# Kernel tuning notes

Hardware: AMD Instinct MI355X
Metric: run time of the kernel (lower is better)

## Reference

```python
import jax, jax.numpy as jnp
import numpy as np

WAVE_LEN = 1000.0

def rank_embedding(rank_dim, feat_dim):
    half = feat_dim // 2
    dim_mat = jnp.arange(half, dtype=jnp.float32) / half
    inv = 1.0 / jnp.power(WAVE_LEN, dim_mat)            # [half]
    mul = jnp.arange(rank_dim, dtype=jnp.float32)[:, None] * inv[None, :]  # [K, half]
    return jnp.concatenate([jnp.sin(mul), jnp.cos(mul)], axis=-1)          # [K, feat_dim]

def setup_inputs() -> dict:
    key = jax.random.key(0)
    ks = jax.random.split(key, 16)
    K, NS, NC, D, DF, H, DK = 2048, 18, 19, 1024, 128, 16, 64
    s = 0.02
    return {
        "size_scores": jax.random.normal(ks[0], (1, K, NS), jnp.float32),
        "size_residuals_normalized": jax.random.normal(ks[1], (1, K, NS, 3), jnp.float32),
        "sem_cls_scores": jax.random.normal(ks[2], (K, NC), jnp.float32),
        "appearance_features": jax.random.normal(ks[3], (K, D), jnp.float32),
        "mean_size_arr": jax.random.uniform(ks[4], (NS, 3), jnp.float32, 0.1, 1.0),
        "w_rank": jax.random.normal(ks[5], (D, DF), jnp.float32) * s,
        "b_rank": jnp.zeros((DF,), jnp.float32),
        "w_roi": jax.random.normal(ks[6], (D, DF), jnp.float32) * s,
        "b_roi": jnp.zeros((DF,), jnp.float32),
        "Wq": jax.random.normal(ks[7], (H, DF, DK), jnp.float32) * s,
        "Wk": jax.random.normal(ks[8], (H, DF, DK), jnp.float32) * s,
        "Wv": jax.random.normal(ks[9], (H, D, DK), jnp.float32) * s,
        "w_logit": jax.random.normal(ks[10], (D, 1), jnp.float32) * s,
        "b_logit": jnp.zeros((1,), jnp.float32),
    }

def reference(size_scores, size_residuals_normalized, sem_cls_scores,
              appearance_features, mean_size_arr,
              w_rank, b_rank, w_roi, b_roi, Wq, Wk, Wv, w_logit, b_logit):
    K, D = appearance_features.shape
    # --- predicted box size: gather residual for argmax size class ---
    pred_size_class = jnp.argmax(size_scores, axis=-1)                     # [1,K]
    size_residuals = size_residuals_normalized * mean_size_arr[None, None] # [1,K,NS,3]
    pred_size_residual = jnp.take_along_axis(
        size_residuals, pred_size_class[..., None, None], axis=2)[:, :, 0, :]  # [1,K,3]
    psc = pred_size_class[0]                                               # [K]
    box_size = mean_size_arr[psc] + pred_size_residual[0]                  # [K,3]
    # --- semantic class prob ---
    prob_all = jax.nn.softmax(sem_cls_scores, axis=-1)                     # [K,NC]
    prob = jnp.max(prob_all, axis=-1)                                      # [K]
    prob_argmax = jnp.argmax(prob_all, axis=-1)                            # [K]
    cls_bbox = box_size                                                    # [K,3]
    # --- background masking (jit-friendly analog of nonzero filtering):
    # background (class 0) proposals get key -1 so they sort to the end with score 0.
    fg = prob_argmax > 0
    sort_key = jnp.where(fg, prob, -1.0)
    order = jnp.argsort(-sort_key)                                         # descending
    sorted_prob = jnp.where(fg[order], prob[order], 0.0)                   # [K]
    sorted_labels = prob_argmax[order]                                     # [K]
    sorted_cls_bboxes = cls_bbox[order]                                    # [K,3]
    sorted_features = appearance_features[order]                           # [K,D]
    # --- rank embedding + roi embedding ---
    emb = rank_embedding(K, D)                                             # [K,D]
    nms_rank = emb @ w_rank + b_rank                                       # [K,DF]
    roi = sorted_features @ w_roi + b_roi                                  # [K,DF]
    e = nms_rank + roi                                                     # [K,DF]
    # --- relation-module self-attention: Q/K from embedding, V from features ---
    dk = Wq.shape[-1]
    q = jnp.einsum('kd,hde->hke', e, Wq)                                   # [H,K,dk]
    k = jnp.einsum('kd,hde->hke', e, Wk)
    scores = jnp.einsum('hke,hme->hkm', q, k) / jnp.sqrt(jnp.float32(dk))  # [H,K,K]
    attn = jax.nn.softmax(scores, axis=-1)
    v = jnp.einsum('kf,hfe->hke', sorted_features, Wv)                     # [H,K,dk]
    o = jnp.einsum('hkm,hme->hke', attn, v)                                # [H,K,dk]
    o = jnp.transpose(o, (1, 0, 2)).reshape(K, -1)                         # [K,D]
    attn_out = sorted_features + o                                         # residual
    # --- nms logit ---
    logit = attn_out @ w_logit + b_logit                                   # [K,1]
    s1 = jax.nn.sigmoid(logit).reshape(-1)
    nms_scores = s1 * sorted_prob
    return nms_scores, sorted_labels - 1, sorted_cls_bboxes
```

## Files before the change

kernel.cpp:

```cpp
#include <hip/hip_runtime.h>

#define KP 2048
#define DD 1024
#define DF 128
#define NH 16
#define DKK 64
#define NSS 18
#define NCC 19
#define NCH 2
#define CHUNK 1024
#define SPLK 16

typedef __attribute__((ext_vector_type(8))) short short8;
typedef __attribute__((ext_vector_type(4))) short short4_t;
typedef __attribute__((ext_vector_type(4))) float f32x4;

__device__ __forceinline__ short f2bf(float x){
    unsigned u = __float_as_uint(x);
    u += 0x7fffu + ((u >> 16) & 1u);
    return (short)(u >> 16);
}

__device__ __forceinline__ void gl2lds16(const void* g, void* l){
    __builtin_amdgcn_global_load_lds((const __attribute__((address_space(1))) void*)g,
                                     (__attribute__((address_space(3))) void*)l, 16, 0, 0);
}

__global__ __launch_bounds__(256) void prep_convw_kernel(const float* __restrict__ size_scores,
        const float* __restrict__ srn, const float* __restrict__ sem,
        const float* __restrict__ mean,
        const float* __restrict__ w_rank, const float* __restrict__ w_roi,
        const float* __restrict__ Wq, const float* __restrict__ Wk,
        const float* __restrict__ Wv, const float* __restrict__ w_logit,
        float* __restrict__ box, int* __restrict__ label,
        double* __restrict__ probd, double* __restrict__ keyd,
        short* __restrict__ wcat, short* __restrict__ qkT, short* __restrict__ uT){
    int bid = blockIdx.x, t = threadIdx.x;
    if (bid < 8){
        int k = bid * 256 + t;
        const float* ss = size_scores + k * NSS;
        int psc = 0; float bs = ss[0];
        for (int s = 1; s < NSS; s++){ float v = ss[s]; if (v > bs){ bs = v; psc = s; } }
        for (int c = 0; c < 3; c++){
            float m = mean[psc * 3 + c];
            float r = srn[k * (NSS * 3) + psc * 3 + c];
            box[k * 3 + c] = m + r * m;
        }
        const float* cs = sem + k * NCC;
        double mx = (double)cs[0]; int lab = 0;
        for (int c = 1; c < NCC; c++){ double v = (double)cs[c]; if (v > mx){ mx = v; lab = c; } }
        double sum = 0.0;
        for (int c = 0; c < NCC; c++) sum += exp((double)cs[c] - mx);
        probd[k] = 1.0 / sum;
        label[k] = lab;
        keyd[k]  = (lab > 0) ? (1.0 / sum) : -1.0;
        return;
    }
    int b = bid - 8;
    if (b >= 128){
        int i = b - 128;
        int h = i >> 2;
        int f = ((i & 3) << 8) + t;
        const float* wv = Wv + (size_t)h * DD * DKK + (size_t)f * DKK;
        const float* wlh = w_logit + h * DKK;
        float s = 0.f;
        #pragma unroll
        for (int e = 0; e < DKK; e++) s += wv[e] * wlh[e];
        uT[h * DD + f] = f2bf(s);
        return;
    }
    __shared__ float tile[64][65];
    const float* src; short* dst; int sstride, dstride, r0, c0, doff;
    float scale = 1.0f;
    if (b < 32){        src = w_rank; dst = wcat; sstride = DF; dstride = 2048;
                        r0 = (b >> 1) * 64; c0 = (b & 1) * 64; doff = 0; }
    else if (b < 64){   int i = b - 32; src = w_roi; dst = wcat; sstride = DF; dstride = 2048;
                        r0 = (i >> 1) * 64; c0 = (i & 1) * 64; doff = 1024; }
    else if (b < 96){   int i = b - 64; int h = i >> 1;
                        src = Wq + (size_t)h * DF * DKK; dst = qkT + (size_t)h * DKK * DF;
                        sstride = DKK; dstride = DF; r0 = (i & 1) * 64; c0 = 0; doff = 0;
                        scale = 0.125f; }
    else {              int i = b - 96; int h = i >> 1;
                        src = Wk + (size_t)h * DF * DKK; dst = qkT + (size_t)(1024 + h * DKK) * DF;
                        sstride = DKK; dstride = DF; r0 = (i & 1) * 64; c0 = 0; doff = 0; }
    int tx = t & 63, ty = t >> 6;
    #pragma unroll
    for (int pp = 0; pp < 16; pp++){
        int r = pp * 4 + ty;
        tile[r][tx] = src[(size_t)(r0 + r) * sstride + c0 + tx];
    }
    __syncthreads();
    #pragma unroll
    for (int pp = 0; pp < 16; pp++){
        int r = pp * 4 + ty;
        dst[(size_t)(c0 + r) * dstride + doff + r0 + tx] = f2bf(tile[tx][r] * scale);
    }
}

__global__ __launch_bounds__(256) void rank_af_kernel(const double* __restrict__ keyd,
        const int* __restrict__ label, const double* __restrict__ probd,
        const float* __restrict__ box, const float* __restrict__ app,
        const float* __restrict__ w_logit,
        int* __restrict__ order, float* __restrict__ sprob, float* __restrict__ dotl,
        short* __restrict__ af, unsigned* __restrict__ cnt, float* __restrict__ out){
    int i = blockIdx.x, t = threadIdx.x;
    if (i < 16 && t == 0) cnt[i] = 0;
    __shared__ int redi[4];
    __shared__ float redf[4];
    __shared__ int rks;
    double ki = keyd[i];
    const double2* k2 = (const double2*)keyd;
    int r = 0;
    #pragma unroll
    for (int pp = 0; pp < KP / 2 / 256; pp++){
        int idx2 = pp * 256 + t;
        double2 kj = k2[idx2];
        int j0 = idx2 * 2;
        r += (int)(kj.x > ki) + (int)((kj.x == ki) & (j0 < i));
        r += (int)(kj.y > ki) + (int)((kj.y == ki) & (j0 + 1 < i));
    }
    #pragma unroll
    for (int off = 32; off > 0; off >>= 1) r += __shfl_down(r, off);
    if ((t & 63) == 0) redi[t >> 6] = r;
    __syncthreads();
    if (t == 0){
        int rk = redi[0] + redi[1] + redi[2] + redi[3];
        rks = rk;
        order[rk] = i;
        sprob[rk] = (label[i] > 0) ? (float)probd[i] : 0.f;
        out[KP + rk] = (float)(label[i] - 1);
        out[2 * KP + 3 * rk + 0] = box[i * 3 + 0];
        out[2 * KP + 3 * rk + 1] = box[i * 3 + 1];
        out[2 * KP + 3 * rk + 2] = box[i * 3 + 2];
    }
    __syncthreads();
    int pos = rks;
    float4 v = ((const float4*)(app + (size_t)i * DD))[t];
    float4 wv = ((const float4*)w_logit)[t];
    short4_t gg = { f2bf(v.x), f2bf(v.y), f2bf(v.z), f2bf(v.w) };
    *(short4_t*)(af + (size_t)pos * 2048 + 1024 + t * 4) = gg;
    float partial = v.x * wv.x + v.y * wv.y + v.z * wv.z + v.w * wv.w;
    #pragma unroll
    for (int off = 32; off > 0; off >>= 1) partial += __shfl_down(partial, off);
    if ((t & 63) == 0) redf[t >> 6] = partial;
    short4_t e;
    #pragma unroll
    for (int ii = 0; ii < 4; ii++){
        int j = t * 4 + ii, jj = j & 511;
        float inv = exp2f(-(float)jj * 0.0194644224310197f);
        float arg = (float)pos * inv;
        e[ii] = f2bf((j < 512) ? __sinf(arg) : __cosf(arg));
    }
    *(short4_t*)(af + (size_t)pos * 2048 + t * 4) = e;
    __syncthreads();
    if (t == 0) dotl[pos] = redf[0] + redf[1] + redf[2] + redf[3];
}

__global__ __launch_bounds__(256) void gemm_lds(const short* __restrict__ A,
                                                const short* __restrict__ BT,
                                                void* __restrict__ C,
                                                int lda, int ldb, int N,
                                                int klen, size_t slabstride, int mode){
    int w = threadIdx.x >> 6, lane = threadIdx.x & 63;
    int quad = lane >> 4, l16 = lane & 15;
    int m0 = blockIdx.x * 64, n0 = blockIdx.y * 64;
    int kb = blockIdx.z * klen;

    __shared__ __align__(16) short alds[64 * 64];
    __shared__ __align__(16) short blds[64 * 64];

    int p0 = w * 64 + lane;
    int r0 = p0 >> 3, q0 = ((p0 & 7) ^ (r0 & 7)) * 8;
    int p1 = p0 + 256;
    int r1 = p1 >> 3, q1 = ((p1 & 7) ^ (r1 & 7)) * 8;
    short* adst0 = alds + w * 512;
    short* adst1 = alds + 2048 + w * 512;
    short* bdst0 = blds + w * 512;
    short* bdst1 = blds + 2048 + w * 512;
    const short* asrc0 = A + (size_t)(m0 + r0) * lda + kb + q0;
    const short* asrc1 = A + (size_t)(m0 + r1) * lda + kb + q1;
    const short* bsrc0 = BT + (size_t)(n0 + r0) * ldb + kb + q0;
    const short* bsrc1 = BT + (size_t)(n0 + r1) * ldb + kb + q1;

    f32x4 acc[4];
    for (int c = 0; c < 4; c++) acc[c] = (f32x4){0.f, 0.f, 0.f, 0.f};

    for (int kt = 0; kt < klen; kt += 64){
        __syncthreads();
        gl2lds16(asrc0 + kt, adst0);
        gl2lds16(asrc1 + kt, adst1);
        gl2lds16(bsrc0 + kt, bdst0);
        gl2lds16(bsrc1 + kt, bdst1);
        __syncthreads();
        int arow = w * 16 + l16;
        #pragma unroll
        for (int s = 0; s < 2; s++){
            short8 a = *(const short8*)(alds + arow * 64 + (((s * 4 + quad) ^ (l16 & 7)) * 8));
            #pragma unroll
            for (int c = 0; c < 4; c++){
                int brow = c * 16 + l16;
                short8 b = *(const short8*)(blds + brow * 64 + (((s * 4 + quad) ^ (l16 & 7)) * 8));
                acc[c] = __builtin_amdgcn_mfma_f32_16x16x32_bf16(a, b, acc[c], 0, 0, 0);
            }
        }
    }
    int mrow = m0 + w * 16 + quad * 4;
    #pragma unroll
    for (int c = 0; c < 4; c++){
        #pragma unroll
        for (int r = 0; r < 4; r++){
            size_t idx = (size_t)(mrow + r) * N + n0 + c * 16 + l16;
            if (mode == 2) ((short*)C)[idx] = f2bf(acc[c][r]);
            else ((float*)C + (size_t)blockIdx.z * slabstride)[idx] = acc[c][r];
        }
    }
}

__global__ __launch_bounds__(256) void comb_vw_kernel(const float* __restrict__ es,
        const float* __restrict__ b_rank, const float* __restrict__ b_roi,
        const short* __restrict__ af, const short* __restrict__ uT,
        short* __restrict__ e_bf, float* __restrict__ vwT){
    int bid = blockIdx.x, t = threadIdx.x;
    if (bid < 256){
        int base = (bid * 256 + t) * 4;
        int n = base & (DF - 1);
        float4 s = *(const float4*)(es + base);
        #pragma unroll
        for (int c = 1; c < SPLK; c++){
            float4 tt = *(const float4*)(es + (size_t)c * KP * DF + base);
            s.x += tt.x; s.y += tt.y; s.z += tt.z; s.w += tt.w;
        }
        float4 br = *(const float4*)(b_rank + n);
        float4 bo = *(const float4*)(b_roi + n);
        short4_t o = { f2bf(s.x + br.x + bo.x), f2bf(s.y + br.y + bo.y),
                       f2bf(s.z + br.z + bo.z), f2bf(s.w + br.w + bo.w) };
        *(short4_t*)(e_bf + base) = o;
    } else {
        int vb = bid - 256;
        int w = t >> 6, lane = t & 63, quad = lane >> 4, l16 = lane & 15;
        int m0 = vb * 64 + w * 16;
        f32x4 acc = (f32x4){0.f, 0.f, 0.f, 0.f};
        const short* arow = af + (size_t)(m0 + l16) * 2048 + 1024 + quad * 8;
        const short* brow = uT + (size_t)l16 * DD + quad * 8;
        for (int k0 = 0; k0 < DD; k0 += 32){
            short8 a = *(const short8*)(arow + k0);
            short8 b = *(const short8*)(brow + k0);
            acc = __builtin_amdgcn_mfma_f32_16x16x32_bf16(a, b, acc, 0, 0, 0);
        }
        #pragma unroll
        for (int r = 0; r < 4; r++)
            vwT[(size_t)l16 * KP + m0 + quad * 4 + r] = acc[r];
    }
}

__global__ __launch_bounds__(256, 4) void attn_final_kernel(const short* __restrict__ qk,
        const float* __restrict__ vwT, const float* __restrict__ dotl,
        const float* __restrict__ sprob, const float* __restrict__ b_logit,
        float* __restrict__ pl, float* __restrict__ pwl,
        unsigned* __restrict__ cnt, float* __restrict__ out){
    int qt = blockIdx.x, h = blockIdx.y, ch = blockIdx.z;
    int t = threadIdx.x;
    int w = t >> 6, lane = t & 63, quad = lane >> 4, l16 = lane & 15;
    int qb = qt * 128;

    __shared__ __align__(16) short klds[64 * 64];
    __shared__ int lastf;

    short8 aq[2][2];
    #pragma unroll
    for (int tt = 0; tt < 2; tt++){
        const short* qrow = qk + (size_t)(qb + tt * 64 + w * 16 + l16) * 2048 + h * DKK;
        aq[tt][0] = *(const short8*)(qrow + quad * 8);
        aq[tt][1] = *(const short8*)(qrow + 32 + quad * 8);
    }
    float lpart[2][4] = {{0.f,0.f,0.f,0.f},{0.f,0.f,0.f,0.f}};
    float wpart[2][4] = {{0.f,0.f,0.f,0.f},{0.f,0.f,0.f,0.f}};

    int seg0 = w * 128 + lane;
    int row0 = seg0 >> 3, c80 = (seg0 & 7) ^ (row0 & 7);
    int seg1 = seg0 + 64;
    int row1 = seg1 >> 3, c81 = (seg1 & 7) ^ (row1 & 7);
    short* kl0 = klds + (size_t)(w * 128) * 8;
    short* kl1 = klds + (size_t)(w * 128 + 64) * 8;

    for (int m0 = ch * CHUNK; m0 < (ch + 1) * CHUNK; m0 += 64){
        __syncthreads();
        gl2lds16(qk + (size_t)(m0 + row0) * 2048 + 1024 + h * DKK + c80 * 8, kl0);
        gl2lds16(qk + (size_t)(m0 + row1) * 2048 + 1024 + h * DKK + c81 * 8, kl1);
        float vwv[4];
        #pragma unroll
        for (int c = 0; c < 4; c++)
            vwv[c] = vwT[(size_t)h * KP + m0 + c * 16 + l16];
        __syncthreads();

        #pragma unroll
        for (int tt = 0; tt < 2; tt++){
            #pragma unroll
            for (int c = 0; c < 4; c++){
                int r = c * 16 + l16, sw = r & 7;
                short8 b0 = *(const short8*)(klds + r * 64 + (quad ^ sw) * 8);
                short8 b1 = *(const short8*)(klds + r * 64 + ((quad + 4) ^ sw) * 8);
                f32x4 acc = (f32x4){0.f, 0.f, 0.f, 0.f};
                acc = __builtin_amdgcn_mfma_f32_16x16x32_bf16(aq[tt][0], b0, acc, 0, 0, 0);
                acc = __builtin_amdgcn_mfma_f32_16x16x32_bf16(aq[tt][1], b1, acc, 0, 0, 0);
                #pragma unroll
                for (int rr = 0; rr < 4; rr++){
                    float e = __expf(acc[rr]);
                    lpart[tt][rr] += e;
                    wpart[tt][rr] += e * vwv[c];
                }
            }
        }
    }

    #pragma unroll
    for (int tt = 0; tt < 2; tt++){
        #pragma unroll
        for (int rr = 0; rr < 4; rr++){
            float v = lpart[tt][rr], x = wpart[tt][rr];
            v += __shfl_xor(v, 1); x += __shfl_xor(x, 1);
            v += __shfl_xor(v, 2); x += __shfl_xor(x, 2);
            v += __shfl_xor(v, 4); x += __shfl_xor(x, 4);
            v += __shfl_xor(v, 8); x += __shfl_xor(x, 8);
            lpart[tt][rr] = v; wpart[tt][rr] = x;
        }
        if (l16 == 0){
            int qr0 = qb + tt * 64 + w * 16;
            #pragma unroll
            for (int rr = 0; rr < 4; rr++){
                size_t idx = ((size_t)ch * NH + h) * KP + qr0 + quad * 4 + rr;
                __hip_atomic_store(pl + idx,  lpart[tt][rr], __ATOMIC_RELAXED, __HIP_MEMORY_SCOPE_AGENT);
                __hip_atomic_store(pwl + idx, wpart[tt][rr], __ATOMIC_RELAXED, __HIP_MEMORY_SCOPE_AGENT);
            }
        }
    }
    __syncthreads();
    if (t == 0){
        __threadfence();
        unsigned old = __hip_atomic_fetch_add(cnt + qt, 1u, __ATOMIC_ACQ_REL, __HIP_MEMORY_SCOPE_AGENT);
        lastf = (old == 31);
    }
    __syncthreads();
    if (lastf){
        __threadfence();
        if (t < 128){
            int pos = qb + t;
            float logit = dotl[pos] + b_logit[0];
            #pragma unroll
            for (int hh = 0; hh < NH; hh++){
                size_t i0 = ((size_t)0 * NH + hh) * KP + pos;
                size_t i1 = ((size_t)1 * NH + hh) * KP + pos;
                float l = __hip_atomic_load(pl + i0, __ATOMIC_RELAXED, __HIP_MEMORY_SCOPE_AGENT)
                        + __hip_atomic_load(pl + i1, __ATOMIC_RELAXED, __HIP_MEMORY_SCOPE_AGENT);
                float x = __hip_atomic_load(pwl + i0, __ATOMIC_RELAXED, __HIP_MEMORY_SCOPE_AGENT)
                        + __hip_atomic_load(pwl + i1, __ATOMIC_RELAXED, __HIP_MEMORY_SCOPE_AGENT);
                logit += x / l;
            }
            float s1 = 1.f / (1.f + __expf(-logit));
            out[pos] = s1 * sprob[pos];
        }
    }
}

extern "C" void kernel_launch(void* const* d_in, const int* in_sizes, int n_in,
                              void* d_out, int out_size, void* d_ws, size_t ws_size,
                              hipStream_t stream){
    (void)in_sizes; (void)n_in; (void)out_size; (void)ws_size;
    const float* size_scores = (const float*)d_in[0];
    const float* srn     = (const float*)d_in[1];
    const float* sem     = (const float*)d_in[2];
    const float* app     = (const float*)d_in[3];
    const float* mean    = (const float*)d_in[4];
    const float* w_rank  = (const float*)d_in[5];
    const float* b_rank  = (const float*)d_in[6];
    const float* w_roi   = (const float*)d_in[7];
    const float* b_roi   = (const float*)d_in[8];
    const float* Wq      = (const float*)d_in[9];
    const float* Wk      = (const float*)d_in[10];
    const float* Wv      = (const float*)d_in[11];
    const float* w_logit = (const float*)d_in[12];
    const float* b_logit = (const float*)d_in[13];
    float* out = (float*)d_out;

    char* ws = (char*)d_ws;
    size_t off = 0;
    auto alloc = [&](size_t n) -> char* {
        char* pp = ws + off;
        off = (off + n + 255) & ~(size_t)255;
        return pp;
    };
    float*    box   = (float*)   alloc((size_t)KP * 3 * 4);
    int*      label = (int*)     alloc((size_t)KP * 4);
    double*   probd = (double*)  alloc((size_t)KP * 8);
    double*   keyd  = (double*)  alloc((size_t)KP * 8);
    int*      order = (int*)     alloc((size_t)KP * 4);
    float*    sprob = (float*)   alloc((size_t)KP * 4);
    float*    dotl  = (float*)   alloc((size_t)KP * 4);
    unsigned* cnt   = (unsigned*)alloc(16 * 4);
    short*    wcat  = (short*)   alloc((size_t)DF * 2048 * 2);
    short*    qkT   = (short*)   alloc((size_t)2048 * DF * 2);
    short*    uT    = (short*)   alloc((size_t)NH * DD * 2);
    short*    e_bf  = (short*)   alloc((size_t)KP * DF * 2);
    short*    qk_bf = (short*)   alloc((size_t)KP * 2048 * 2);
    float*    vwT   = (float*)   alloc((size_t)NH * KP * 4);
    float*    pl    = (float*)   alloc((size_t)NCH * NH * KP * 4);
    float*    pwl   = (float*)   alloc((size_t)NCH * NH * KP * 4);
    short*    af    = (short*)   alloc((size_t)KP * 2048 * 2);
    float*    es    = (float*)   alloc((size_t)SPLK * KP * DF * 4);

    prep_convw_kernel<<<200, 256, 0, stream>>>(size_scores, srn, sem, mean,
        w_rank, w_roi, Wq, Wk, Wv, w_logit, box, label, probd, keyd, wcat, qkT, uT);
    rank_af_kernel<<<KP, 256, 0, stream>>>(keyd, label, probd, box, app, w_logit,
        order, sprob, dotl, af, cnt, out);
    gemm_lds<<<dim3(32, 2, SPLK), 256, 0, stream>>>(af, wcat, es, 2048, 2048, DF,
        2048 / SPLK, (size_t)KP * DF, 0);
    comb_vw_kernel<<<288, 256, 0, stream>>>(es, b_rank, b_roi, af, uT, e_bf, vwT);
    gemm_lds<<<dim3(32, 32, 1), 256, 0, stream>>>(e_bf, qkT, qk_bf, DF, DF, 2048, DF, 0, 2);
    attn_final_kernel<<<dim3(16, NH, NCH), 256, 0, stream>>>(qk_bf, vwT, dotl, sprob,
        b_logit, pl, pwl, cnt, out);
}
```

Measured before the change: 154.3 us.

## Split attention key chunks wider, halve split-K, move final reduction to separate kernel

```diff
diff --git a/kernel.cpp b/kernel.cpp
--- a/kernel.cpp
+++ b/kernel.cpp
@@ -7,9 +7,9 @@
 #define DKK 64
 #define NSS 18
 #define NCC 19
-#define NCH 2
-#define CHUNK 1024
-#define SPLK 16
+#define NCH 4
+#define CHUNK 512
+#define SPLK 8
 
 typedef __attribute__((ext_vector_type(8))) short short8;
 typedef __attribute__((ext_vector_type(4))) short short4_t;
@@ -101,10 +101,9 @@
         const int* __restrict__ label, const double* __restrict__ probd,
         const float* __restrict__ box, const float* __restrict__ app,
         const float* __restrict__ w_logit,
-        int* __restrict__ order, float* __restrict__ sprob, float* __restrict__ dotl,
-        short* __restrict__ af, unsigned* __restrict__ cnt, float* __restrict__ out){
+        float* __restrict__ sprob, float* __restrict__ dotl,
+        short* __restrict__ af, float* __restrict__ out){
     int i = blockIdx.x, t = threadIdx.x;
-    if (i < 16 && t == 0) cnt[i] = 0;
     __shared__ int redi[4];
     __shared__ float redf[4];
     __shared__ int rks;
@@ -126,7 +125,6 @@
     if (t == 0){
         int rk = redi[0] + redi[1] + redi[2] + redi[3];
         rks = rk;
-        order[rk] = i;
         sprob[rk] = (label[i] > 0) ? (float)probd[i] : 0.f;
         out[KP + rk] = (float)(label[i] - 1);
         out[2 * KP + 3 * rk + 0] = box[i * 3 + 0];
@@ -253,18 +251,15 @@
     }
 }
 
-__global__ __launch_bounds__(256, 4) void attn_final_kernel(const short* __restrict__ qk,
-        const float* __restrict__ vwT, const float* __restrict__ dotl,
-        const float* __restrict__ sprob, const float* __restrict__ b_logit,
-        float* __restrict__ pl, float* __restrict__ pwl,
-        unsigned* __restrict__ cnt, float* __restrict__ out){
+__global__ __launch_bounds__(256, 4) void attn_kernel(const short* __restrict__ qk,
+        const float* __restrict__ vwT,
+        float* __restrict__ pl, float* __restrict__ pwl){
     int qt = blockIdx.x, h = blockIdx.y, ch = blockIdx.z;
     int t = threadIdx.x;
     int w = t >> 6, lane = t & 63, quad = lane >> 4, l16 = lane & 15;
     int qb = qt * 128;
 
     __shared__ __align__(16) short klds[64 * 64];
-    __shared__ int lastf;
 
     short8 aq[2][2];
     #pragma unroll
@@ -329,37 +324,31 @@
             #pragma unroll
             for (int rr = 0; rr < 4; rr++){
                 size_t idx = ((size_t)ch * NH + h) * KP + qr0 + quad * 4 + rr;
-                __hip_atomic_store(pl + idx,  lpart[tt][rr], __ATOMIC_RELAXED, __HIP_MEMORY_SCOPE_AGENT);
-                __hip_atomic_store(pwl + idx, wpart[tt][rr], __ATOMIC_RELAXED, __HIP_MEMORY_SCOPE_AGENT);
+                pl[idx]  = lpart[tt][rr];
+                pwl[idx] = wpart[tt][rr];
             }
         }
     }
-    __syncthreads();
-    if (t == 0){
-        __threadfence();
-        unsigned old = __hip_atomic_fetch_add(cnt + qt, 1u, __ATOMIC_ACQ_REL, __HIP_MEMORY_SCOPE_AGENT);
-        lastf = (old == 31);
-    }
-    __syncthreads();
-    if (lastf){
-        __threadfence();
-        if (t < 128){
-            int pos = qb + t;
-            float logit = dotl[pos] + b_logit[0];
-            #pragma unroll
-            for (int hh = 0; hh < NH; hh++){
-                size_t i0 = ((size_t)0 * NH + hh) * KP + pos;
-                size_t i1 = ((size_t)1 * NH + hh) * KP + pos;
-                float l = __hip_atomic_load(pl + i0, __ATOMIC_RELAXED, __HIP_MEMORY_SCOPE_AGENT)
-                        + __hip_atomic_load(pl + i1, __ATOMIC_RELAXED, __HIP_MEMORY_SCOPE_AGENT);
-                float x = __hip_atomic_load(pwl + i0, __ATOMIC_RELAXED, __HIP_MEMORY_SCOPE_AGENT)
-                        + __hip_atomic_load(pwl + i1, __ATOMIC_RELAXED, __HIP_MEMORY_SCOPE_AGENT);
-                logit += x / l;
-            }
-            float s1 = 1.f / (1.f + __expf(-logit));
-            out[pos] = s1 * sprob[pos];
-        }
-    }
+}
+
+__global__ __launch_bounds__(256) void final_kernel(const float* __restrict__ dotl,
+        const float* __restrict__ pl, const float* __restrict__ pwl,
+        const float* __restrict__ sprob, const float* __restrict__ b_logit,
+        float* __restrict__ out){
+    int pos = blockIdx.x * 256 + threadIdx.x;
+    float logit = dotl[pos] + b_logit[0];
+    #pragma unroll
+    for (int h = 0; h < NH; h++){
+        float l = 0.f, x = 0.f;
+        #pragma unroll
+        for (int c = 0; c < NCH; c++){
+            size_t idx = ((size_t)c * NH + h) * KP + pos;
+            l += pl[idx]; x += pwl[idx];
+        }
+        logit += x / l;
+    }
+    float s1 = 1.f / (1.f + __expf(-logit));
+    out[pos] = s1 * sprob[pos];
 }
 
 extern "C" void kernel_launch(void* const* d_in, const int* in_sizes, int n_in,
@@ -389,33 +378,31 @@
         off = (off + n + 255) & ~(size_t)255;
         return pp;
     };
-    float*    box   = (float*)   alloc((size_t)KP * 3 * 4);
-    int*      label = (int*)     alloc((size_t)KP * 4);
-    double*   probd = (double*)  alloc((size_t)KP * 8);
-    double*   keyd  = (double*)  alloc((size_t)KP * 8);
-    int*      order = (int*)     alloc((size_t)KP * 4);
-    float*    sprob = (float*)   alloc((size_t)KP * 4);
-    float*    dotl  = (float*)   alloc((size_t)KP * 4);
-    unsigned* cnt   = (unsigned*)alloc(16 * 4);
-    short*    wcat  = (short*)   alloc((size_t)DF * 2048 * 2);
-    short*    qkT   = (short*)   alloc((size_t)2048 * DF * 2);
-    short*    uT    = (short*)   alloc((size_t)NH * DD * 2);
-    short*    e_bf  = (short*)   alloc((size_t)KP * DF * 2);
-    short*    qk_bf = (short*)   alloc((size_t)KP * 2048 * 2);
-    float*    vwT   = (float*)   alloc((size_t)NH * KP * 4);
-    float*    pl    = (float*)   alloc((size_t)NCH * NH * KP * 4);
-    float*    pwl   = (float*)   alloc((size_t)NCH * NH * KP * 4);
-    short*    af    = (short*)   alloc((size_t)KP * 2048 * 2);
-    float*    es    = (float*)   alloc((size_t)SPLK * KP * DF * 4);
+    float*  box   = (float*)  alloc((size_t)KP * 3 * 4);
+    int*    label = (int*)    alloc((size_t)KP * 4);
+    double* probd = (double*) alloc((size_t)KP * 8);
+    double* keyd  = (double*) alloc((size_t)KP * 8);
+    float*  sprob = (float*)  alloc((size_t)KP * 4);
+    float*  dotl  = (float*)  alloc((size_t)KP * 4);
+    short*  wcat  = (short*)  alloc((size_t)DF * 2048 * 2);
+    short*  qkT   = (short*)  alloc((size_t)2048 * DF * 2);
+    short*  uT    = (short*)  alloc((size_t)NH * DD * 2);
+    short*  e_bf  = (short*)  alloc((size_t)KP * DF * 2);
+    short*  qk_bf = (short*)  alloc((size_t)KP * 2048 * 2);
+    float*  vwT   = (float*)  alloc((size_t)NH * KP * 4);
+    float*  pl    = (float*)  alloc((size_t)NCH * NH * KP * 4);
+    float*  pwl   = (float*)  alloc((size_t)NCH * NH * KP * 4);
+    short*  af    = (short*)  alloc((size_t)KP * 2048 * 2);
+    float*  es    = (float*)  alloc((size_t)SPLK * KP * DF * 4);
 
     prep_convw_kernel<<<200, 256, 0, stream>>>(size_scores, srn, sem, mean,
         w_rank, w_roi, Wq, Wk, Wv, w_logit, box, label, probd, keyd, wcat, qkT, uT);
     rank_af_kernel<<<KP, 256, 0, stream>>>(keyd, label, probd, box, app, w_logit,
-        order, sprob, dotl, af, cnt, out);
+        sprob, dotl, af, out);
     gemm_lds<<<dim3(32, 2, SPLK), 256, 0, stream>>>(af, wcat, es, 2048, 2048, DF,
         2048 / SPLK, (size_t)KP * DF, 0);
     comb_vw_kernel<<<288, 256, 0, stream>>>(es, b_rank, b_roi, af, uT, e_bf, vwT);
     gemm_lds<<<dim3(32, 32, 1), 256, 0, stream>>>(e_bf, qkT, qk_bf, DF, DF, 2048, DF, 0, 2);
-    attn_final_kernel<<<dim3(16, NH, NCH), 256, 0, stream>>>(qk_bf, vwT, dotl, sprob,
-        b_logit, pl, pwl, cnt, out);
-}
+    attn_kernel<<<dim3(KP / 128, NH, NCH), 256, 0, stream>>>(qk_bf, vwT, pl, pwl);
+    final_kernel<<<KP / 256, 256, 0, stream>>>(dotl, pl, pwl, sprob, b_logit, out);
+}
```

Result: faster. 139.9 us (-9.3%).
